# Optimization experiments

Hardware: AMD Instinct MI355X
Metric: run time of the kernel (lower is better)

Reference implementation:

```python
import jax, jax.numpy as jnp
import numpy as np

PI = 3.141592653589793


def setup_inputs() -> dict:
    key = jax.random.key(0)
    k1, k2, k3, k4 = jax.random.split(key, 4)
    B, N, C, H, V = 4, 4096, 128, 8, 16
    inputs = jax.random.normal(k1, (B, N, C), dtype=jnp.float32)
    dist = jax.random.uniform(k2, (N, N), dtype=jnp.float32)
    r = jax.random.normal(k3, (H, 1, 1), dtype=jnp.float32)
    weight = jax.random.normal(k4, (H, C, V), dtype=jnp.float32)
    return {"inputs": inputs, "dist": dist, "r": r, "weight": weight, "locality": 64}


def reference(inputs, dist, r, weight, locality):
    # scaled_dist: (H, N, N) -- learnable bandwidth per head via tan/sin transform
    scaled = dist[None, :, :] * jnp.tan(0.25 * PI * (1.0 + jnp.sin(r)))
    # quantile-based local masking along last axis (linear interpolation,
    # matching tfp.stats.percentile with interpolation='linear')
    mask = jnp.percentile(scaled, float(locality), axis=-1, keepdims=True, method="linear")
    fmax = jnp.finfo(jnp.float32).max
    scaled = jnp.where(scaled <= mask, scaled, fmax)
    # softmax over key axis of -scaled_dist (masked entries -> -fmax -> ~0 weight)
    att = jax.nn.softmax(-scaled, axis=-1)  # (H, N, N)
    # per-head value projection: (B,N,C) x (H,C,V) -> (B,H,N,V)
    value = jnp.einsum("bnj,hjk->bhnk", inputs, weight)
    # attention aggregation: (H,N,N) x (B,H,N,V) -> (B,H,N,V)
    concat = jnp.einsum("hnj,bhjd->bhnd", att, value)
    B, H, N, V = concat.shape
    concat = concat.transpose(0, 2, 1, 3).reshape(B, N, H * V)  # (B, N, hid_dim)
    # tf.keras.activations.gelu defaults to exact (non-approximate) gelu
    return jax.nn.gelu(concat, approximate=False)
```

## Files before the change

### kernel.cpp

```cpp
#include <hip/hip_runtime.h>
#include <hip/hip_bf16.h>
#include <math.h>

#define NN 4096
#define NC 128
#define NH 8
#define NV 16
#define NB 4
#define BD 64

typedef _Float16 half8 __attribute__((ext_vector_type(8)));
typedef float floatx4 __attribute__((ext_vector_type(4)));

__device__ __forceinline__ int get_loc(const int* locp){
    int lr = locp[0];
    return (lr >= 0 && lr <= 100) ? lr : 64;
}
__device__ __forceinline__ float head_scale(const float* rr, int h){
    float ts = tanf(0.78539816339744831f * (1.0f + sinf(rr[h])));
    if (!(ts > 0.f)) ts = (ts == 0.f) ? 1e-20f : 1e20f;
    if (ts > 1e20f) ts = 1e20f;
    return ts;
}
__device__ __forceinline__ void lds_barrier(){
    __asm__ __volatile__("s_waitcnt lgkmcnt(0)\n\ts_barrier" ::: "memory");
}

__global__ __launch_bounds__(256) void k_rowstats(const float* __restrict__ dist,
                                                  const int* __restrict__ locp,
                                                  float* __restrict__ Kval,
                                                  float* __restrict__ xminp){
    __shared__ unsigned int hist[4][256];
    __shared__ float cand[1024];
    __shared__ unsigned int cnt, selb_s, basec_s, xminu;
    const int i = blockIdx.x, t = threadIdx.x;
    const int wv = t >> 6, lane = t & 63;
    const int loc = get_loc(locp);
    const unsigned int rank = (unsigned int)(((long long)loc * (NN - 1)) / 100) + 1u;

    float v[16];
    const float4* rp = (const float4*)(dist + (size_t)i * NN);
#pragma unroll
    for (int k = 0; k < 4; k++){
        float4 x4 = rp[k * 256 + t];
        v[4*k+0] = x4.x; v[4*k+1] = x4.y; v[4*k+2] = x4.z; v[4*k+3] = x4.w;
    }
    for (int k = t; k < 1024; k += 256) ((unsigned int*)hist)[k] = 0;
    if (t == 0){ cnt = 0; selb_s = 255u; basec_s = 0u; xminu = 0xFFFFFFFFu; }
    __syncthreads();

    float lmin = 1e30f;
#pragma unroll
    for (int u = 0; u < 16; u++){
        float x = v[u];
        lmin = fminf(lmin, x);
        int b = (int)(x * 256.0f); b = b < 0 ? 0 : (b > 255 ? 255 : b);
        atomicAdd(&hist[wv][b], 1u);
    }
#pragma unroll
    for (int off = 1; off < 64; off <<= 1) lmin = fminf(lmin, __shfl_xor(lmin, off));
    if (lane == 0) atomicMin(&xminu, __float_as_uint(lmin));
    __syncthreads();

    if (t < 64){
        unsigned int lp[4];
        unsigned int run = 0;
#pragma unroll
        for (int q = 0; q < 4; q++){
            int b = 4 * t + q;
            run += hist[0][b] + hist[1][b] + hist[2][b] + hist[3][b];
            lp[q] = run;
        }
        unsigned int incl = run;
#pragma unroll
        for (int d = 1; d < 64; d <<= 1){
            unsigned int y = __shfl_up(incl, d);
            if (t >= d) incl += y;
        }
        unsigned int excl = incl - run;
        if (excl < rank && rank <= incl){
#pragma unroll
            for (int q = 0; q < 4; q++){
                if (excl + lp[q] >= rank){
                    selb_s  = (unsigned int)(4 * t + q);
                    basec_s = excl + (q ? lp[q-1] : 0u);
                    break;
                }
            }
        }
    }
    __syncthreads();
    const unsigned int sb = selb_s;
    if (t == 0) Kval[i] = ((float)sb + 1.0f) * 0.00390625f;
#pragma unroll
    for (int u = 0; u < 16; u++){
        float x = v[u];
        int b = (int)(x * 256.0f); b = b < 0 ? 0 : (b > 255 ? 255 : b);
        if ((unsigned int)b == sb){
            unsigned int idx = atomicAdd(&cnt, 1u);
            if (idx < 1024u) cand[idx] = x;
        }
    }
    __syncthreads();
    const unsigned int n = cnt > 1024u ? 1024u : cnt;
    const unsigned int need = rank - basec_s;
    for (unsigned int c0 = t; c0 < n; c0 += 256){
        float x = cand[c0];
        unsigned int lt = 0, le = 0;
        for (unsigned int k2 = 0; k2 < n; k2++){
            float y = cand[k2];
            lt += (y < x); le += (y <= x);
        }
        if (lt < need && need <= le) Kval[i] = x;
    }
    if (t == 0) xminp[i] = __uint_as_float(xminu);
}

__global__ __launch_bounds__(256) void k_value(const float* __restrict__ in,
                                               const float* __restrict__ wgt,
                                               _Float16* __restrict__ val_t){
    __shared__ float insh[NC * 65];
    __shared__ float wsh[NC * NV];
    const int j0 = blockIdx.x * 16;
    const int h  = blockIdx.y;
    const int t  = threadIdx.x;

    for (int k = t; k < NC * NV; k += 256) wsh[k] = wgt[h * NC * NV + k];
#pragma unroll
    for (int k = 0; k < 32; k++){
        int idx = k * 256 + t;
        int p = idx >> 7, c = idx & 127;
        int b = p >> 4, jl = p & 15;
        insh[c * 65 + jl * 4 + b] = in[((size_t)b * NN + j0 + jl) * NC + c];
    }
    __syncthreads();

    const int r = t & 63, dq = t >> 6;
    const int jl = r >> 2, b = r & 3;
    float a0 = 0.f, a1 = 0.f, a2 = 0.f, a3 = 0.f;
#pragma unroll 8
    for (int c = 0; c < NC; c++){
        float x = insh[c * 65 + r];
        float4 w4 = *(const float4*)&wsh[c * NV + dq * 4];
        a0 = fmaf(x, w4.x, a0);
        a1 = fmaf(x, w4.y, a1);
        a2 = fmaf(x, w4.z, a2);
        a3 = fmaf(x, w4.w, a3);
    }
    const size_t base = ((size_t)(h * BD + b * NV + dq * 4)) * NN + j0 + jl;
    val_t[base         ] = (_Float16)a0;
    val_t[base + NN    ] = (_Float16)a1;
    val_t[base + 2 * NN] = (_Float16)a2;
    val_t[base + 3 * NN] = (_Float16)a3;
}

__global__ __launch_bounds__(256) void k_att(const float* __restrict__ dist,
                                             const float* __restrict__ rr,
                                             const _Float16* __restrict__ val_t,
                                             const float* __restrict__ Kvalp,
                                             const float* __restrict__ xminp,
                                             float* __restrict__ out){
    __shared__ alignas(16) _Float16 wtile[2][32 * 72];
    __shared__ alignas(16) _Float16 vtile[2][64 * 72];

    const int i0 = blockIdx.x * 32;
    const int h  = blockIdx.y;
    const int t  = threadIdx.x;
    const int lane = t & 63, wv = t >> 6;
    const float ts  = head_scale(rr, h);
    const float ts2 = ts * 1.44269504088896f;

    const int il = t >> 3, jq = t & 7;
    const int vrow = t >> 3, vpart = t & 7;
    const float kvi  = Kvalp[i0 + il];
    const float txmi = ts2 * xminp[i0 + il];
    const float nts2 = -ts2;

    const float* dp = dist + (size_t)(i0 + il) * NN + jq * 8;
    const _Float16* vp0 = val_t + (size_t)(h * BD + vrow) * NN + vpart * 8;
    const _Float16* vp1 = vp0 + (size_t)32 * NN;

    half8 ones;
#pragma unroll
    for (int u = 0; u < 8; u++) ones[u] = (_Float16)1.0f;

    floatx4 acc0 = (floatx4){0.f,0.f,0.f,0.f};
    floatx4 acc1 = (floatx4){0.f,0.f,0.f,0.f};
    floatx4 accs = (floatx4){0.f,0.f,0.f,0.f};

    const int is16 = (wv & 1) * 16;
    const int bh   = (wv >> 1) * 32;
    const int aoff  = (is16 + (lane & 15)) * 72 + (lane >> 4) * 8;
    const int boff0 = (bh + (lane & 15)) * 72 + (lane >> 4) * 8;
    const int boff1 = boff0 + 16 * 72;
    const int voff0 = vrow * 72 + vpart * 8;
    const int voff1 = (vrow + 32) * 72 + vpart * 8;
    const int woff  = il * 72 + jq * 8;

    uint4 pv0 = *(const uint4*)vp0;  vp0 += 64;
    uint4 pv1 = *(const uint4*)vp1;  vp1 += 64;
    float4 pd0 = *(const float4*)dp;
    float4 pd1 = *(const float4*)(dp + 4);  dp += 64;

    {
        *(uint4*)&vtile[0][voff0] = pv0;
        *(uint4*)&vtile[0][voff1] = pv1;
        const float dd[8] = {pd0.x,pd0.y,pd0.z,pd0.w,pd1.x,pd1.y,pd1.z,pd1.w};
        half8 hw;
#pragma unroll
        for (int u = 0; u < 8; u++){
            float e = __builtin_amdgcn_exp2f(fmaf(nts2, dd[u], txmi));
            hw[u] = (_Float16)((dd[u] <= kvi) ? e : 0.f);
        }
        *(half8*)&wtile[0][woff] = hw;
    }

    for (int jt = 0; jt < NN / 64; jt++){
        const int cur = jt & 1;
        const bool more = (jt != NN / 64 - 1);
        if (more){
            pv0 = *(const uint4*)vp0;  vp0 += 64;
            pv1 = *(const uint4*)vp1;  vp1 += 64;
            pd0 = *(const float4*)dp;
            pd1 = *(const float4*)(dp + 4);  dp += 64;
        }
        lds_barrier();

#pragma unroll
        for (int kc = 0; kc < 2; kc++){
            half8 af = *(const half8*)&wtile[cur][aoff + kc * 32];
            half8 b0 = *(const half8*)&vtile[cur][boff0 + kc * 32];
            half8 b1 = *(const half8*)&vtile[cur][boff1 + kc * 32];
            acc0 = __builtin_amdgcn_mfma_f32_16x16x32_f16(af, b0, acc0, 0, 0, 0);
            acc1 = __builtin_amdgcn_mfma_f32_16x16x32_f16(af, b1, acc1, 0, 0, 0);
            accs = __builtin_amdgcn_mfma_f32_16x16x32_f16(af, ones, accs, 0, 0, 0);
        }

        if (more){
            const int nxt = 1 - cur;
            *(uint4*)&vtile[nxt][voff0] = pv0;
            *(uint4*)&vtile[nxt][voff1] = pv1;
            const float dd[8] = {pd0.x,pd0.y,pd0.z,pd0.w,pd1.x,pd1.y,pd1.z,pd1.w};
            half8 hw;
#pragma unroll
            for (int u = 0; u < 8; u++){
                float e = __builtin_amdgcn_exp2f(fmaf(nts2, dd[u], txmi));
                hw[u] = (_Float16)((dd[u] <= kvi) ? e : 0.f);
            }
            *(half8*)&wtile[nxt][woff] = hw;
        }
    }

    const int m0 = (lane >> 4) * 4;
    const int d  = lane & 15;
#pragma unroll
    for (int r4 = 0; r4 < 4; r4++){
        const int iloc = is16 + m0 + r4;
        const float inv_s = 1.0f / fmaxf(accs[r4], 1e-30f);
#pragma unroll
        for (int nt = 0; nt < 2; nt++){
            const int b = (wv >> 1) * 2 + nt;
            float c = acc0[r4], c1 = acc1[r4];
            float cc = (nt == 0 ? c : c1) * inv_s;
            float g = 0.5f * cc * (1.0f + erff(cc * 0.70710678118654752f));
            out[((size_t)b * NN + i0 + iloc) * (NH * NV) + h * NV + d] = g;
        }
    }
}

extern "C" void kernel_launch(void* const* d_in, const int* in_sizes, int n_in,
                              void* d_out, int out_size, void* d_ws, size_t ws_size,
                              hipStream_t stream) {
    const float* in   = (const float*)d_in[0];
    const float* dist = (const float*)d_in[1];
    const float* r    = (const float*)d_in[2];
    const float* wgt  = (const float*)d_in[3];
    const int*   loc  = (const int*)d_in[4];
    float* out = (float*)d_out;

    float* Kval = (float*)d_ws;
    float* xmin = Kval + NN;
    _Float16* val_t = (_Float16*)((char*)d_ws + 2 * (size_t)NN * sizeof(float));

    k_rowstats<<<NN, 256, 0, stream>>>(dist, loc, Kval, xmin);
    k_value<<<dim3(NN / 16, NH), 256, 0, stream>>>(in, wgt, val_t);
    k_att<<<dim3(NN / 32, NH), 256, 0, stream>>>(dist, r, val_t, Kval, xmin, out);
}
```

Measured before the change: 185.5 us.

## Deepen attention prefetch to two tiles, remap blocks per XCD, pack fp16 conversion

Keeps two j-tiles of global loads in flight by unrolling the main loop by two with separate register sets, so load latency is hidden more deeply. It also remaps the linear block index so consecutive blocks on each XCD share query rows across heads, improving L2 reuse of dist rows. The mask is now applied before exp2 by clamping the exponent, and pairs are packed with cvt_pkrtz to reduce conversion instructions. The cost is higher register pressure and round-toward-zero conversion instead of round-to-nearest.

```diff
diff --git a/kernel.cpp b/kernel.cpp
--- a/kernel.cpp
+++ b/kernel.cpp
@@ -10,6 +10,7 @@
 #define BD 64
 
 typedef _Float16 half8 __attribute__((ext_vector_type(8)));
+typedef __fp16  fp16x2 __attribute__((ext_vector_type(2)));
 typedef float floatx4 __attribute__((ext_vector_type(4)));
 
 __device__ __forceinline__ int get_loc(const int* locp){
@@ -163,9 +164,13 @@
     __shared__ alignas(16) _Float16 wtile[2][32 * 72];
     __shared__ alignas(16) _Float16 vtile[2][64 * 72];
 
-    const int i0 = blockIdx.x * 32;
-    const int h  = blockIdx.y;
-    const int t  = threadIdx.x;
+    const int l   = blockIdx.x + (NN / 32) * blockIdx.y;
+    const int xcd = l & 7;
+    const int s   = l >> 3;
+    const int i0  = (xcd * 16 + (s >> 3)) * 32;
+    const int h   = s & 7;
+
+    const int t = threadIdx.x;
     const int lane = t & 63, wv = t >> 6;
     const float ts  = head_scale(rr, h);
     const float ts2 = ts * 1.44269504088896f;
@@ -176,13 +181,13 @@
     const float txmi = ts2 * xminp[i0 + il];
     const float nts2 = -ts2;
 
+    half8 ones;
+#pragma unroll
+    for (int u = 0; u < 8; u++) ones[u] = (_Float16)1.0f;
+
     const float* dp = dist + (size_t)(i0 + il) * NN + jq * 8;
     const _Float16* vp0 = val_t + (size_t)(h * BD + vrow) * NN + vpart * 8;
     const _Float16* vp1 = vp0 + (size_t)32 * NN;
-
-    half8 ones;
-#pragma unroll
-    for (int u = 0; u < 8; u++) ones[u] = (_Float16)1.0f;
 
     floatx4 acc0 = (floatx4){0.f,0.f,0.f,0.f};
     floatx4 acc1 = (floatx4){0.f,0.f,0.f,0.f};
@@ -197,59 +202,65 @@
     const int voff1 = (vrow + 32) * 72 + vpart * 8;
     const int woff  = il * 72 + jq * 8;
 
-    uint4 pv0 = *(const uint4*)vp0;  vp0 += 64;
-    uint4 pv1 = *(const uint4*)vp1;  vp1 += 64;
-    float4 pd0 = *(const float4*)dp;
-    float4 pd1 = *(const float4*)(dp + 4);  dp += 64;
-
-    {
-        *(uint4*)&vtile[0][voff0] = pv0;
-        *(uint4*)&vtile[0][voff1] = pv1;
-        const float dd[8] = {pd0.x,pd0.y,pd0.z,pd0.w,pd1.x,pd1.y,pd1.z,pd1.w};
-        half8 hw;
-#pragma unroll
-        for (int u = 0; u < 8; u++){
-            float e = __builtin_amdgcn_exp2f(fmaf(nts2, dd[u], txmi));
-            hw[u] = (_Float16)((dd[u] <= kvi) ? e : 0.f);
-        }
-        *(half8*)&wtile[0][woff] = hw;
-    }
-
-    for (int jt = 0; jt < NN / 64; jt++){
-        const int cur = jt & 1;
-        const bool more = (jt != NN / 64 - 1);
-        if (more){
-            pv0 = *(const uint4*)vp0;  vp0 += 64;
-            pv1 = *(const uint4*)vp1;  vp1 += 64;
-            pd0 = *(const float4*)dp;
-            pd1 = *(const float4*)(dp + 4);  dp += 64;
-        }
+    uint4  Av0, Av1, Bv0, Bv1;
+    float4 Ad0, Ad1, Bd0, Bd1;
+
+#define LOADSET(V0, V1, D0, D1) do{                                          \
+        V0 = *(const uint4*)vp0;  vp0 += 64;                                 \
+        V1 = *(const uint4*)vp1;  vp1 += 64;                                 \
+        D0 = *(const float4*)dp;                                             \
+        D1 = *(const float4*)(dp + 4);  dp += 64; }while(0)
+
+#define STAGE(BUF, V0, V1, D0, D1) do{                                       \
+        *(uint4*)&vtile[BUF][voff0] = V0;                                    \
+        *(uint4*)&vtile[BUF][voff1] = V1;                                    \
+        const float dd_[8] = {D0.x,D0.y,D0.z,D0.w,D1.x,D1.y,D1.z,D1.w};      \
+        union { half8 h8; fp16x2 h2[4]; } uu_;                               \
+        _Pragma("unroll")                                                    \
+        for (int u_ = 0; u_ < 4; u_++){                                      \
+            float a0_ = fmaf(nts2, dd_[2*u_  ], txmi);                       \
+            float a1_ = fmaf(nts2, dd_[2*u_+1], txmi);                       \
+            a0_ = (dd_[2*u_  ] <= kvi) ? a0_ : -20000.0f;                    \
+            a1_ = (dd_[2*u_+1] <= kvi) ? a1_ : -20000.0f;                    \
+            uu_.h2[u_] = __builtin_amdgcn_cvt_pkrtz(                         \
+                __builtin_amdgcn_exp2f(a0_), __builtin_amdgcn_exp2f(a1_));   \
+        }                                                                    \
+        *(half8*)&wtile[BUF][woff] = uu_.h8; }while(0)
+
+#define MFMA_T(BUF) do{                                                      \
+        _Pragma("unroll")                                                    \
+        for (int kc_ = 0; kc_ < 2; kc_++){                                   \
+            half8 af = *(const half8*)&wtile[BUF][aoff  + kc_ * 32];         \
+            half8 b0 = *(const half8*)&vtile[BUF][boff0 + kc_ * 32];         \
+            half8 b1 = *(const half8*)&vtile[BUF][boff1 + kc_ * 32];         \
+            acc0 = __builtin_amdgcn_mfma_f32_16x16x32_f16(af, b0, acc0, 0, 0, 0); \
+            acc1 = __builtin_amdgcn_mfma_f32_16x16x32_f16(af, b1, acc1, 0, 0, 0); \
+            accs = __builtin_amdgcn_mfma_f32_16x16x32_f16(af, ones, accs, 0, 0, 0); \
+        } }while(0)
+
+    LOADSET(Av0, Av1, Ad0, Ad1);
+    LOADSET(Bv0, Bv1, Bd0, Bd1);
+    STAGE(0, Av0, Av1, Ad0, Ad1);
+
+    for (int jp = 0; jp < 31; jp++){
+        LOADSET(Av0, Av1, Ad0, Ad1);
         lds_barrier();
-
-#pragma unroll
-        for (int kc = 0; kc < 2; kc++){
-            half8 af = *(const half8*)&wtile[cur][aoff + kc * 32];
-            half8 b0 = *(const half8*)&vtile[cur][boff0 + kc * 32];
-            half8 b1 = *(const half8*)&vtile[cur][boff1 + kc * 32];
-            acc0 = __builtin_amdgcn_mfma_f32_16x16x32_f16(af, b0, acc0, 0, 0, 0);
-            acc1 = __builtin_amdgcn_mfma_f32_16x16x32_f16(af, b1, acc1, 0, 0, 0);
-            accs = __builtin_amdgcn_mfma_f32_16x16x32_f16(af, ones, accs, 0, 0, 0);
-        }
-
-        if (more){
-            const int nxt = 1 - cur;
-            *(uint4*)&vtile[nxt][voff0] = pv0;
-            *(uint4*)&vtile[nxt][voff1] = pv1;
-            const float dd[8] = {pd0.x,pd0.y,pd0.z,pd0.w,pd1.x,pd1.y,pd1.z,pd1.w};
-            half8 hw;
-#pragma unroll
-            for (int u = 0; u < 8; u++){
-                float e = __builtin_amdgcn_exp2f(fmaf(nts2, dd[u], txmi));
-                hw[u] = (_Float16)((dd[u] <= kvi) ? e : 0.f);
-            }
-            *(half8*)&wtile[nxt][woff] = hw;
-        }
-    }
+        MFMA_T(0);
+        STAGE(1, Bv0, Bv1, Bd0, Bd1);
+        LOADSET(Bv0, Bv1, Bd0, Bd1);
+        lds_barrier();
+        MFMA_T(1);
+        STAGE(0, Av0, Av1, Ad0, Ad1);
+    }
+    lds_barrier();
+    MFMA_T(0);
+    STAGE(1, Bv0, Bv1, Bd0, Bd1);
+    lds_barrier();
+    MFMA_T(1);
+
+#undef LOADSET
+#undef STAGE
+#undef MFMA_T
 
     const int m0 = (lane >> 4) * 4;
     const int d  = lane & 15;
```

New measurement: 177.6 us. -4.3%, faster.
